# Performance work log

Measured on AMD Instinct MI355X. Metric: run time of the kernel, lower is better.

## Reference

```python
import jax, jax.numpy as jnp
import numpy as np

EPS = 1e-5
B, C_IN, T_IN = 512, 12, 5000
NF, HID, LAT = 32, 64, 32


def setup_inputs() -> dict:
    key = jax.random.key(0)
    ks = jax.random.split(key, 12)
    inp = {
        "x": jax.random.normal(ks[0], (B, C_IN, T_IN), dtype=jnp.float32),
        # conv stack
        "conv1_w": jax.random.normal(ks[1], (32, C_IN, 50), dtype=jnp.float32) * 0.05,
        "conv1_b": jnp.zeros((32,), dtype=jnp.float32),
        "bn1_g": jnp.ones((32,), dtype=jnp.float32),
        "bn1_b": jnp.zeros((32,), dtype=jnp.float32),
        "conv2_w": jax.random.normal(ks[2], (NF, 32, 25), dtype=jnp.float32) * 0.05,
        "conv2_b": jnp.zeros((NF,), dtype=jnp.float32),
        "bn2_g": jnp.ones((NF,), dtype=jnp.float32),
        "bn2_b": jnp.zeros((NF,), dtype=jnp.float32),
        # input projection + layernorm
        "proj_w": jax.random.normal(ks[3], (LAT, NF), dtype=jnp.float32) * 0.1,
        "proj_b": jnp.zeros((LAT,), dtype=jnp.float32),
        "ln_g": jnp.ones((LAT,), dtype=jnp.float32),
        "ln_b": jnp.zeros((LAT,), dtype=jnp.float32),
        # PLRNN recurrence params
        "A": jnp.eye(LAT, dtype=jnp.float32) * 0.9,
        "W": jax.random.normal(ks[4], (LAT, HID), dtype=jnp.float32) * 0.1,
        "h_bias": jnp.zeros((HID,), dtype=jnp.float32),
        # output projection
        "out_w": jax.random.normal(ks[5], (LAT, LAT), dtype=jnp.float32) * 0.1,
        "out_b": jnp.zeros((LAT,), dtype=jnp.float32),
    }
    return inp


def _conv1d(x, w, b, stride):
    # x: [B, C, T], w: [O, I, K]
    y = jax.lax.conv_general_dilated(
        x, w, window_strides=(stride,), padding="VALID",
        dimension_numbers=("NCH", "OIH", "NCH"))
    return y + b[None, :, None]


def _batchnorm_train(x, g, b):
    # training-mode BN over (batch, time) per channel; x: [B, C, T]
    mean = jnp.mean(x, axis=(0, 2), keepdims=True)
    var = jnp.mean((x - mean) ** 2, axis=(0, 2), keepdims=True)
    return (x - mean) * jax.lax.rsqrt(var + EPS) * g[None, :, None] + b[None, :, None]


def _layernorm(x, g, b):
    mean = jnp.mean(x, axis=-1, keepdims=True)
    var = jnp.mean((x - mean) ** 2, axis=-1, keepdims=True)
    return (x - mean) * jax.lax.rsqrt(var + EPS) * g + b


def reference(x, conv1_w, conv1_b, bn1_g, bn1_b, conv2_w, conv2_b, bn2_g, bn2_b,
              proj_w, proj_b, ln_g, ln_b, A, W, h_bias, out_w, out_b):
    # conv front-end
    y = jax.nn.relu(_batchnorm_train(_conv1d(x, conv1_w, conv1_b, 10), bn1_g, bn1_b))
    y = jax.nn.relu(_batchnorm_train(_conv1d(y, conv2_w, conv2_b, 5), bn2_g, bn2_b))
    y = jnp.transpose(y, (0, 2, 1))  # [B, T, NF], T = 95

    # input projection + LN, vectorized over all timesteps
    xt = _layernorm(jnp.einsum("btf,lf->btl", y, proj_w) + proj_b, ln_g, ln_b)  # [B, T, L]
    xs = jnp.transpose(xt, (1, 0, 2))  # [T, B, L] for scan

    def step(h, x_t):
        # h: [B, L]
        linear = h @ A.T
        nonlinear = jax.nn.relu(h @ W + h_bias) @ W.T
        h_new = linear + nonlinear + x_t
        return h_new, h_new

    h0 = jnp.zeros((x.shape[0], A.shape[0]), dtype=x.dtype)
    _, outputs = jax.lax.scan(step, h0, xs)  # [T, B, L]

    pooled = jnp.mean(outputs, axis=0)  # [B, L]
    return pooled @ out_w.T + out_b
```

## Files before the change

kernel.cpp:

```cpp
#include <hip/hip_runtime.h>
#include <stdint.h>

#define NB    512
#define CIN   12
#define TIN   5000
#define T1    496
#define T2    95

#define OFS_STATS 0
#define OFS_W1P   256
#define OFS_W2P   19456
#define OFS_Y1    45056
#define OFS_Y2    8171520

#define GAS __attribute__((address_space(1)))
#define LAS __attribute__((address_space(3)))
#define ASYNC_COPY16(gp, lp) \
    __builtin_amdgcn_global_load_lds((const GAS void*)(gp), (LAS void*)(lp), 16, 0, 0)

__global__ void prep_kernel(const float* __restrict__ w1, const float* __restrict__ w2,
                            float* __restrict__ ws) {
    int idx = blockIdx.x * 256 + threadIdx.x;
    if (idx < 256) ws[idx] = 0.f;
    int j = idx - 256;
    if (j >= 0 && j < 19200) {
        int ic = j / 1600, r = j % 1600, k = r / 32, oc = r % 32;
        ws[OFS_W1P + j] = w1[oc * 600 + ic * 50 + k];
    }
    int j2 = idx - 19456;
    if (j2 >= 0 && j2 < 25600) {
        int ic = j2 / 800, r = j2 % 800, k = r / 32, oc = r % 32;
        ws[OFS_W2P + j2] = w2[oc * 800 + ic * 25 + k];
    }
}

__global__ __launch_bounds__(128, 2) void conv1_kernel(const float* __restrict__ x,
                                                       const float* __restrict__ b1,
                                                       float* __restrict__ ws) {
    const float* w1p = ws + OFS_W1P;
    float* y1 = ws + OFS_Y1;
    float* stats = ws + OFS_STATS;
    int b  = blockIdx.x >> 1;
    int t0 = (blockIdx.x & 1) * 256;
    int tid = threadIdx.x;
    int ocg = tid & 3, tg = tid >> 2;
    int oc0 = ocg * 8;
    int xoff = 10 * tg;

    __shared__ __align__(16) float xs_s[2][2600];
    __shared__ __align__(16) float ws_s[2][1600];
    __shared__ float sred[128];

    float acc[8][8];
#pragma unroll
    for (int a = 0; a < 8; ++a)
#pragma unroll
        for (int c = 0; c < 8; ++c) acc[a][c] = 0.f;

    const float* xb = x + (size_t)b * (CIN * TIN) + t0 * 10;
    const int nchunk = (t0 == 0) ? 650 : 610;
    const int wbase = tid & ~63;

    if (t0 != 0) {
        for (int i = tid; i < 160; i += 128) {
            xs_s[0][2440 + i] = 0.f;
            xs_s[1][2440 + i] = 0.f;
        }
    }

    auto issue = [&](int ic) {
        int buf = ic & 1;
        const float* xg = xb + ic * TIN;
#pragma unroll
        for (int c = 0; c < 6; ++c) {
            int i = c * 128 + tid;
            if (i < nchunk)
                ASYNC_COPY16(xg + 4 * i, &xs_s[buf][4 * (c * 128 + wbase)]);
        }
        const float* wg = w1p + ic * 1600;
#pragma unroll
        for (int c = 0; c < 4; ++c) {
            int i = c * 128 + tid;
            if (i < 400)
                ASYNC_COPY16(wg + 4 * i, &ws_s[buf][4 * (c * 128 + wbase)]);
        }
    };

    issue(0);
    for (int ic = 0; ic < CIN; ++ic) {
        const int cur = ic & 1;
        __syncthreads();
        if (ic + 1 < CIN) issue(ic + 1);

#pragma unroll 1
        for (int m = 0; m < 5; ++m) {
#pragma unroll
            for (int u = 0; u < 5; ++u) {
                const int k = m * 10 + u * 2;
                const float* wr = &ws_s[cur][k * 32 + oc0];
                float4 w00 = *(const float4*)(wr);
                float4 w01 = *(const float4*)(wr + 4);
                float4 w10 = *(const float4*)(wr + 32);
                float4 w11 = *(const float4*)(wr + 36);
                float2 xv[8];
#pragma unroll
                for (int j = 0; j < 8; ++j)
                    xv[j] = *(const float2*)&xs_s[cur][xoff + 320 * j + k];
                float wk[8]  = {w00.x, w00.y, w00.z, w00.w, w01.x, w01.y, w01.z, w01.w};
                float wk1[8] = {w10.x, w10.y, w10.z, w10.w, w11.x, w11.y, w11.z, w11.w};
#pragma unroll
                for (int jo = 0; jo < 8; ++jo)
#pragma unroll
                    for (int j = 0; j < 8; ++j)
                        acc[jo][j] = fmaf(wk1[jo], xv[j].y, fmaf(wk[jo], xv[j].x, acc[jo][j]));
            }
        }
    }

    float bias[8];
#pragma unroll
    for (int jo = 0; jo < 8; ++jo) bias[jo] = b1[oc0 + jo];

    float psum[8], psq[8];
#pragma unroll
    for (int jo = 0; jo < 8; ++jo) { psum[jo] = 0.f; psq[jo] = 0.f; }
#pragma unroll
    for (int jo = 0; jo < 8; ++jo) {
        float* yrow = y1 + (size_t)(b * 32 + oc0 + jo) * T1 + t0 + tg;
#pragma unroll
        for (int j = 0; j < 8; ++j) {
            int trel = tg + 32 * j;
            if (t0 + trel < T1) {
                float v = acc[jo][j] + bias[jo];
                yrow[32 * j] = v;
                psum[jo] += v;
                psq[jo] = fmaf(v, v, psq[jo]);
            }
        }
    }
#pragma unroll
    for (int off = 32; off >= 4; off >>= 1) {
#pragma unroll
        for (int jo = 0; jo < 8; ++jo) {
            psum[jo] += __shfl_down(psum[jo], off, 64);
            psq[jo]  += __shfl_down(psq[jo],  off, 64);
        }
    }
    int lane = tid & 63, wvi = tid >> 6;
    if (lane < 4) {
#pragma unroll
        for (int jo = 0; jo < 8; ++jo) {
            sred[((wvi * 4 + lane) * 8 + jo) * 2 + 0] = psum[jo];
            sred[((wvi * 4 + lane) * 8 + jo) * 2 + 1] = psq[jo];
        }
    }
    __syncthreads();
    if (tid < 64) {
        int oc = tid >> 1, which = tid & 1;
        int og = oc >> 3, jo = oc & 7;
        float v = sred[((0 * 4 + og) * 8 + jo) * 2 + which] +
                  sred[((1 * 4 + og) * 8 + jo) * 2 + which];
        atomicAdd(&stats[which * 32 + oc], v);
    }
}

__global__ __launch_bounds__(256, 2) void conv2bn_kernel(const float* __restrict__ g1,
                                                         const float* __restrict__ be1,
                                                         const float* __restrict__ b2,
                                                         float* __restrict__ ws) {
    const float* w2p = ws + OFS_W2P;
    const float* y1 = ws + OFS_Y1;
    float* y2 = ws + OFS_Y2;
    float* stats = ws + OFS_STATS;
    int b = blockIdx.x, tid = threadIdx.x;
    int ocg = tid & 7, tg = tid >> 3;
    int oc0 = ocg * 4;

    __shared__ float s1s[32], sh1s[32];
    __shared__ __align__(16) float a1s[512];
    __shared__ __align__(16) float w2s[800];
    __shared__ float sred[256];

    float acc[4][3];
#pragma unroll
    for (int a = 0; a < 4; ++a)
#pragma unroll
        for (int c = 0; c < 3; ++c) acc[a][c] = 0.f;

    if (tid < 32) {
        float mean = stats[tid] * (1.f / 253952.f);
        float var  = stats[32 + tid] * (1.f / 253952.f) - mean * mean;
        float s = g1[tid] * rsqrtf(var + 1e-5f);
        s1s[tid] = s;
        sh1s[tid] = be1[tid] - mean * s;
    }

    float4 pa, pw2;
    auto fetch = [&](int ic) {
        if (tid < 124) pa  = *(const float4*)(y1 + (size_t)(b * 32 + ic) * T1 + 4 * tid);
        if (tid < 200) pw2 = *(const float4*)(w2p + ic * 800 + 4 * tid);
    };
    fetch(0);
    __syncthreads();

#pragma unroll 1
    for (int ic = 0; ic < 32; ++ic) {
        float s1 = s1s[ic], sh1 = sh1s[ic];
        if (tid < 124) {
            float4 v = pa;
            v.x = fmaxf(fmaf(v.x, s1, sh1), 0.f);
            v.y = fmaxf(fmaf(v.y, s1, sh1), 0.f);
            v.z = fmaxf(fmaf(v.z, s1, sh1), 0.f);
            v.w = fmaxf(fmaf(v.w, s1, sh1), 0.f);
            *(float4*)&a1s[4 * tid] = v;
        }
        if (tid < 200) *(float4*)&w2s[4 * tid] = pw2;
        if (ic + 1 < 32) fetch(ic + 1);
        __builtin_amdgcn_sched_barrier(0);
        __syncthreads();

#pragma unroll
        for (int kp = 0; kp < 12; ++kp) {
            const int k = kp * 2;
            float4 wA = *(const float4*)&w2s[k * 32 + oc0];
            float4 wB = *(const float4*)&w2s[(k + 1) * 32 + oc0];
            float x0[3], x1[3];
#pragma unroll
            for (int jt = 0; jt < 3; ++jt) {
                int a = 15 * tg + 5 * jt + k;
                x0[jt] = a1s[a]; x1[jt] = a1s[a + 1];
            }
            float wk[4]  = {wA.x, wA.y, wA.z, wA.w};
            float wk1[4] = {wB.x, wB.y, wB.z, wB.w};
#pragma unroll
            for (int jo = 0; jo < 4; ++jo)
#pragma unroll
                for (int jt = 0; jt < 3; ++jt)
                    acc[jo][jt] = fmaf(wk1[jo], x1[jt], fmaf(wk[jo], x0[jt], acc[jo][jt]));
        }
        {
            float4 wT = *(const float4*)&w2s[24 * 32 + oc0];
            float wt[4] = {wT.x, wT.y, wT.z, wT.w};
#pragma unroll
            for (int jt = 0; jt < 3; ++jt) {
                float xt_ = a1s[15 * tg + 5 * jt + 24];
#pragma unroll
                for (int jo = 0; jo < 4; ++jo) acc[jo][jt] = fmaf(wt[jo], xt_, acc[jo][jt]);
            }
        }
        __syncthreads();
    }

    float bias[4];
#pragma unroll
    for (int jo = 0; jo < 4; ++jo) bias[jo] = b2[oc0 + jo];

    float psum[4], psq[4];
#pragma unroll
    for (int jo = 0; jo < 4; ++jo) {
        float s = 0.f, q = 0.f;
#pragma unroll
        for (int jt = 0; jt < 3; ++jt) {
            int t2 = 3 * tg + jt;
            if (t2 < T2) {
                float v = acc[jo][jt] + bias[jo];
                y2[(size_t)b * 3040 + (oc0 + jo) * T2 + t2] = v;
                s += v; q = fmaf(v, v, q);
            }
        }
        psum[jo] = s; psq[jo] = q;
    }
#pragma unroll
    for (int off = 32; off >= 8; off >>= 1) {
#pragma unroll
        for (int jo = 0; jo < 4; ++jo) {
            psum[jo] += __shfl_down(psum[jo], off, 64);
            psq[jo]  += __shfl_down(psq[jo],  off, 64);
        }
    }
    int lane = tid & 63, wvi = tid >> 6;
    if (lane < 8) {
#pragma unroll
        for (int jo = 0; jo < 4; ++jo) {
            sred[((wvi * 8 + lane) * 4 + jo) * 2 + 0] = psum[jo];
            sred[((wvi * 8 + lane) * 4 + jo) * 2 + 1] = psq[jo];
        }
    }
    __syncthreads();
    if (tid < 64) {
        int oc = tid >> 1, which = tid & 1;
        int og = oc >> 2, jo = oc & 3;
        float v = 0.f;
#pragma unroll
        for (int w = 0; w < 4; ++w)
            v += sred[((w * 8 + og) * 4 + jo) * 2 + which];
        atomicAdd(&stats[64 + which * 32 + oc], v);
    }
}

__global__ __launch_bounds__(256, 2) void projscan_kernel(const float* __restrict__ g2,
                                                          const float* __restrict__ be2,
                                                          const float* __restrict__ pw,
                                                          const float* __restrict__ pb,
                                                          const float* __restrict__ lng,
                                                          const float* __restrict__ lnb,
                                                          const float* __restrict__ Am,
                                                          const float* __restrict__ Wm,
                                                          const float* __restrict__ hbp,
                                                          const float* __restrict__ ow,
                                                          const float* __restrict__ ob,
                                                          const float* __restrict__ ws,
                                                          float* __restrict__ out) {
    int b = blockIdx.x, tid = threadIdx.x;
    __shared__ float s2s[32], sh2s[32];
    __shared__ __align__(16) float a2s[3040];
    __shared__ float pws[1056], ows[1056];
    __shared__ __align__(16) float xsl[3135];
    __shared__ __align__(16) float hs[32];
    __shared__ __align__(16) float hds[64];
    const float* stats = ws + OFS_STATS;
    const float* y2b = ws + OFS_Y2 + (size_t)b * 3040;

    if (tid < 32) {
        float mean = stats[64 + tid] * (1.f / 48640.f);
        float var  = stats[96 + tid] * (1.f / 48640.f) - mean * mean;
        float s = g2[tid] * rsqrtf(var + 1e-5f);
        s2s[tid] = s;
        sh2s[tid] = be2[tid] - mean * s;
    }
    for (int i = tid; i < 1024; i += 256) {
        pws[(i >> 5) * 33 + (i & 31)] = pw[i];
        ows[(i >> 5) * 33 + (i & 31)] = ow[i];
    }
    __syncthreads();

    for (int i = tid; i < 760; i += 256) {
        float4 v = *(const float4*)(y2b + 4 * i);
        float r[4] = {v.x, v.y, v.z, v.w};
        float o[4];
#pragma unroll
        for (int e = 0; e < 4; ++e) {
            int idx = 4 * i + e;
            int oc = idx / 95;
            o[e] = fmaxf(fmaf(r[e], s2s[oc], sh2s[oc]), 0.f);
        }
        float4 vv; vv.x = o[0]; vv.y = o[1]; vv.z = o[2]; vv.w = o[3];
        *(float4*)&a2s[4 * i] = vv;
    }
    __syncthreads();

    int l = tid & 31, ts = tid >> 5;
    {
        float pbv = pb[l], lg = lng[l], lb = lnb[l];
        for (int it = 0; it < 12; ++it) {
            int t = ts + 8 * it;
            if (t < T2) {
                float v = pbv;
#pragma unroll
                for (int f = 0; f < 32; ++f)
                    v = fmaf(a2s[f * T2 + t], pws[l * 33 + f], v);
                float sum = v;
#pragma unroll
                for (int off = 16; off >= 1; off >>= 1) sum += __shfl_xor(sum, off, 64);
                float mean = sum * (1.f / 32.f);
                float d = v - mean;
                float q = d * d;
#pragma unroll
                for (int off = 16; off >= 1; off >>= 1) q += __shfl_xor(q, off, 64);
                float o = d * rsqrtf(q * (1.f / 32.f) + 1e-5f) * lg + lb;
                xsl[t * 33 + l] = o;
            }
        }
    }
    __syncthreads();

    if (tid < 64) {
        int lane = tid, half = lane >> 5;
        float Wc[32], WT[32], Ah[16];
#pragma unroll
        for (int j = 0; j < 32; ++j) Wc[j] = Wm[j * 64 + lane];
#pragma unroll
        for (int m = 0; m < 32; ++m) WT[m] = Wm[l * 64 + half * 32 + m];
#pragma unroll
        for (int j = 0; j < 16; ++j) Ah[j] = Am[l * 32 + half * 16 + j];
        float hbv = hbp[lane];
        if (lane < 32) hs[l] = 0.f;
        float xv = xsl[l];
        float pool = 0.f;

        for (int t = 0; t < T2; ++t) {
            float4 hv[8];
#pragma unroll
            for (int q = 0; q < 8; ++q) hv[q] = *(const float4*)&hs[4 * q];
            float a0 = hbv, a1 = 0.f, a2 = 0.f, a3 = 0.f;
#pragma unroll
            for (int q = 0; q < 8; ++q) {
                a0 = fmaf(Wc[4 * q + 0], hv[q].x, a0);
                a1 = fmaf(Wc[4 * q + 1], hv[q].y, a1);
                a2 = fmaf(Wc[4 * q + 2], hv[q].z, a2);
                a3 = fmaf(Wc[4 * q + 3], hv[q].w, a3);
            }
            float hid = fmaxf((a0 + a1) + (a2 + a3), 0.f);
            float4 hl[4];
#pragma unroll
            for (int q = 0; q < 4; ++q) hl[q] = *(const float4*)&hs[half * 16 + 4 * q];
            float l0 = 0.f, l1 = 0.f;
#pragma unroll
            for (int q = 0; q < 4; ++q) {
                l0 = fmaf(Ah[4 * q + 0], hl[q].x, l0);
                l1 = fmaf(Ah[4 * q + 1], hl[q].y, l1);
                l0 = fmaf(Ah[4 * q + 2], hl[q].z, l0);
                l1 = fmaf(Ah[4 * q + 3], hl[q].w, l1);
            }
            float lin = l0 + l1;
            hds[lane] = hid;
            float n0 = 0.f, n1 = 0.f, n2 = 0.f, n3 = 0.f;
#pragma unroll
            for (int q = 0; q < 8; ++q) {
                float4 d4 = *(const float4*)&hds[half * 32 + 4 * q];
                n0 = fmaf(WT[4 * q + 0], d4.x, n0);
                n1 = fmaf(WT[4 * q + 1], d4.y, n1);
                n2 = fmaf(WT[4 * q + 2], d4.z, n2);
                n3 = fmaf(WT[4 * q + 3], d4.w, n3);
            }
            float part = (n0 + n1) + (n2 + n3) + lin;
            part += __shfl_xor(part, 32, 64);
            float hnew = part + xv;
            pool += hnew;
            if (t + 1 < T2) xv = xsl[(t + 1) * 33 + l];
            if (lane < 32) hs[l] = hnew;
        }

        if (lane < 32) hs[l] = pool * (1.f / 95.f);
        if (lane < 32) {
            float4 p0 = *(const float4*)&hs[0];
            float4 p1 = *(const float4*)&hs[4];
            float4 p2 = *(const float4*)&hs[8];
            float4 p3 = *(const float4*)&hs[12];
            float4 p4 = *(const float4*)&hs[16];
            float4 p5 = *(const float4*)&hs[20];
            float4 p6 = *(const float4*)&hs[24];
            float4 p7 = *(const float4*)&hs[28];
            float o = ob[l];
            const float* owr = &ows[l * 33];
            o = fmaf(owr[0],  p0.x, o); o = fmaf(owr[1],  p0.y, o);
            o = fmaf(owr[2],  p0.z, o); o = fmaf(owr[3],  p0.w, o);
            o = fmaf(owr[4],  p1.x, o); o = fmaf(owr[5],  p1.y, o);
            o = fmaf(owr[6],  p1.z, o); o = fmaf(owr[7],  p1.w, o);
            o = fmaf(owr[8],  p2.x, o); o = fmaf(owr[9],  p2.y, o);
            o = fmaf(owr[10], p2.z, o); o = fmaf(owr[11], p2.w, o);
            o = fmaf(owr[12], p3.x, o); o = fmaf(owr[13], p3.y, o);
            o = fmaf(owr[14], p3.z, o); o = fmaf(owr[15], p3.w, o);
            o = fmaf(owr[16], p4.x, o); o = fmaf(owr[17], p4.y, o);
            o = fmaf(owr[18], p4.z, o); o = fmaf(owr[19], p4.w, o);
            o = fmaf(owr[20], p5.x, o); o = fmaf(owr[21], p5.y, o);
            o = fmaf(owr[22], p5.z, o); o = fmaf(owr[23], p5.w, o);
            o = fmaf(owr[24], p6.x, o); o = fmaf(owr[25], p6.y, o);
            o = fmaf(owr[26], p6.z, o); o = fmaf(owr[27], p6.w, o);
            o = fmaf(owr[28], p7.x, o); o = fmaf(owr[29], p7.y, o);
            o = fmaf(owr[30], p7.z, o); o = fmaf(owr[31], p7.w, o);
            out[b * 32 + l] = o;
        }
    }
}

extern "C" void kernel_launch(void* const* d_in, const int* in_sizes, int n_in,
                              void* d_out, int out_size, void* d_ws, size_t ws_size,
                              hipStream_t stream) {
    (void)in_sizes; (void)n_in; (void)out_size; (void)ws_size;
    const float* x   = (const float*)d_in[0];
    const float* w1  = (const float*)d_in[1];
    const float* b1  = (const float*)d_in[2];
    const float* g1  = (const float*)d_in[3];
    const float* be1 = (const float*)d_in[4];
    const float* w2  = (const float*)d_in[5];
    const float* b2  = (const float*)d_in[6];
    const float* g2  = (const float*)d_in[7];
    const float* be2 = (const float*)d_in[8];
    const float* pw  = (const float*)d_in[9];
    const float* pb  = (const float*)d_in[10];
    const float* lng = (const float*)d_in[11];
    const float* lnb = (const float*)d_in[12];
    const float* Am  = (const float*)d_in[13];
    const float* Wm  = (const float*)d_in[14];
    const float* hb  = (const float*)d_in[15];
    const float* ow  = (const float*)d_in[16];
    const float* ob  = (const float*)d_in[17];
    float* ws  = (float*)d_ws;
    float* out = (float*)d_out;

    prep_kernel<<<176, 256, 0, stream>>>(w1, w2, ws);
    conv1_kernel<<<1024, 128, 0, stream>>>(x, b1, ws);
    conv2bn_kernel<<<512, 256, 0, stream>>>(g1, be1, b2, ws);
    projscan_kernel<<<512, 256, 0, stream>>>(g2, be2, pw, pb, lng, lnb,
                                             Am, Wm, hb, ow, ob, ws, out);
}
```

Before: 498.8 us.

## Restructure conv kernels to per-thread time columns with uniform scalar weight loads

Both conv kernels now give each thread one or two time positions and all 32 output channels. Weights are no longer staged through LDS; they are read directly from global memory with wave-uniform addresses that the compiler can turn into scalar loads. conv2 drops to 128 threads, uses async global-to-LDS copies for the input rows, and reduces BN statistics with full-wave shuffles. This removes LDS weight traffic and bank pressure but raises register use (64 accumulators plus 64 partial sums), leaves about a quarter of the threads idle in conv2, and adds more shuffle work.

Measured after the change: 841.9 us. 68.8% more time.

```diff
diff --git a/kernel.cpp b/kernel.cpp
--- a/kernel.cpp
+++ b/kernel.cpp
@@ -37,36 +37,23 @@
 __global__ __launch_bounds__(128, 2) void conv1_kernel(const float* __restrict__ x,
                                                        const float* __restrict__ b1,
                                                        float* __restrict__ ws) {
-    const float* w1p = ws + OFS_W1P;
+    const float* __restrict__ w1p = ws + OFS_W1P;
     float* y1 = ws + OFS_Y1;
     float* stats = ws + OFS_STATS;
     int b  = blockIdx.x >> 1;
     int t0 = (blockIdx.x & 1) * 256;
     int tid = threadIdx.x;
-    int ocg = tid & 3, tg = tid >> 2;
-    int oc0 = ocg * 8;
-    int xoff = 10 * tg;
 
     __shared__ __align__(16) float xs_s[2][2600];
-    __shared__ __align__(16) float ws_s[2][1600];
     __shared__ float sred[128];
 
-    float acc[8][8];
-#pragma unroll
-    for (int a = 0; a < 8; ++a)
-#pragma unroll
-        for (int c = 0; c < 8; ++c) acc[a][c] = 0.f;
+    float acc[32][2];
+#pragma unroll
+    for (int oc = 0; oc < 32; ++oc) { acc[oc][0] = 0.f; acc[oc][1] = 0.f; }
 
     const float* xb = x + (size_t)b * (CIN * TIN) + t0 * 10;
     const int nchunk = (t0 == 0) ? 650 : 610;
     const int wbase = tid & ~63;
-
-    if (t0 != 0) {
-        for (int i = tid; i < 160; i += 128) {
-            xs_s[0][2440 + i] = 0.f;
-            xs_s[1][2440 + i] = 0.f;
-        }
-    }
 
     auto issue = [&](int ic) {
         int buf = ic & 1;
@@ -76,13 +63,6 @@
             int i = c * 128 + tid;
             if (i < nchunk)
                 ASYNC_COPY16(xg + 4 * i, &xs_s[buf][4 * (c * 128 + wbase)]);
-        }
-        const float* wg = w1p + ic * 1600;
-#pragma unroll
-        for (int c = 0; c < 4; ++c) {
-            int i = c * 128 + tid;
-            if (i < 400)
-                ASYNC_COPY16(wg + 4 * i, &ws_s[buf][4 * (c * 128 + wbase)]);
         }
     };
 
@@ -91,101 +71,78 @@
         const int cur = ic & 1;
         __syncthreads();
         if (ic + 1 < CIN) issue(ic + 1);
-
+        const float* __restrict__ wrow = w1p + ic * 1600;
+        const int x0 = 10 * tid;
 #pragma unroll 1
-        for (int m = 0; m < 5; ++m) {
-#pragma unroll
-            for (int u = 0; u < 5; ++u) {
-                const int k = m * 10 + u * 2;
-                const float* wr = &ws_s[cur][k * 32 + oc0];
-                float4 w00 = *(const float4*)(wr);
-                float4 w01 = *(const float4*)(wr + 4);
-                float4 w10 = *(const float4*)(wr + 32);
-                float4 w11 = *(const float4*)(wr + 36);
-                float2 xv[8];
-#pragma unroll
-                for (int j = 0; j < 8; ++j)
-                    xv[j] = *(const float2*)&xs_s[cur][xoff + 320 * j + k];
-                float wk[8]  = {w00.x, w00.y, w00.z, w00.w, w01.x, w01.y, w01.z, w01.w};
-                float wk1[8] = {w10.x, w10.y, w10.z, w10.w, w11.x, w11.y, w11.z, w11.w};
-#pragma unroll
-                for (int jo = 0; jo < 8; ++jo)
-#pragma unroll
-                    for (int j = 0; j < 8; ++j)
-                        acc[jo][j] = fmaf(wk1[jo], xv[j].y, fmaf(wk[jo], xv[j].x, acc[jo][j]));
+        for (int kp = 0; kp < 25; ++kp) {
+            const int k = kp * 2;
+            float2 xv0 = *(const float2*)&xs_s[cur][x0 + k];
+            float2 xv1 = *(const float2*)&xs_s[cur][x0 + 1280 + k];
+            const float* __restrict__ wk = wrow + k * 32;
+#pragma unroll
+            for (int oc = 0; oc < 32; ++oc) {
+                float w0 = wk[oc];
+                float w1v = wk[32 + oc];
+                acc[oc][0] = fmaf(w1v, xv0.y, fmaf(w0, xv0.x, acc[oc][0]));
+                acc[oc][1] = fmaf(w1v, xv1.y, fmaf(w0, xv1.x, acc[oc][1]));
             }
         }
     }
 
-    float bias[8];
-#pragma unroll
-    for (int jo = 0; jo < 8; ++jo) bias[jo] = b1[oc0 + jo];
-
-    float psum[8], psq[8];
-#pragma unroll
-    for (int jo = 0; jo < 8; ++jo) { psum[jo] = 0.f; psq[jo] = 0.f; }
-#pragma unroll
-    for (int jo = 0; jo < 8; ++jo) {
-        float* yrow = y1 + (size_t)(b * 32 + oc0 + jo) * T1 + t0 + tg;
-#pragma unroll
-        for (int j = 0; j < 8; ++j) {
-            int trel = tg + 32 * j;
-            if (t0 + trel < T1) {
-                float v = acc[jo][j] + bias[jo];
-                yrow[32 * j] = v;
-                psum[jo] += v;
-                psq[jo] = fmaf(v, v, psq[jo]);
-            }
-        }
-    }
-#pragma unroll
-    for (int off = 32; off >= 4; off >>= 1) {
-#pragma unroll
-        for (int jo = 0; jo < 8; ++jo) {
-            psum[jo] += __shfl_down(psum[jo], off, 64);
-            psq[jo]  += __shfl_down(psq[jo],  off, 64);
-        }
-    }
-    int lane = tid & 63, wvi = tid >> 6;
-    if (lane < 4) {
-#pragma unroll
-        for (int jo = 0; jo < 8; ++jo) {
-            sred[((wvi * 4 + lane) * 8 + jo) * 2 + 0] = psum[jo];
-            sred[((wvi * 4 + lane) * 8 + jo) * 2 + 1] = psq[jo];
+    bool v1 = (t0 + 128 + tid) < T1;
+    float psum[32], psq[32];
+#pragma unroll
+    for (int oc = 0; oc < 32; ++oc) {
+        float bi = b1[oc];
+        float a0 = acc[oc][0] + bi;
+        float a1v = acc[oc][1] + bi;
+        float* yr = y1 + (size_t)(b * 32 + oc) * T1 + t0 + tid;
+        yr[0] = a0;
+        float s = a0, q = a0 * a0;
+        if (v1) { yr[128] = a1v; s += a1v; q = fmaf(a1v, a1v, q); }
+        psum[oc] = s; psq[oc] = q;
+    }
+#pragma unroll
+    for (int off = 32; off >= 1; off >>= 1) {
+#pragma unroll
+        for (int oc = 0; oc < 32; ++oc) {
+            psum[oc] += __shfl_down(psum[oc], off, 64);
+            psq[oc]  += __shfl_down(psq[oc],  off, 64);
+        }
+    }
+    int lane = tid & 63, wv = tid >> 6;
+    if (lane == 0) {
+#pragma unroll
+        for (int oc = 0; oc < 32; ++oc) {
+            sred[wv * 64 + oc * 2 + 0] = psum[oc];
+            sred[wv * 64 + oc * 2 + 1] = psq[oc];
         }
     }
     __syncthreads();
     if (tid < 64) {
         int oc = tid >> 1, which = tid & 1;
-        int og = oc >> 3, jo = oc & 7;
-        float v = sred[((0 * 4 + og) * 8 + jo) * 2 + which] +
-                  sred[((1 * 4 + og) * 8 + jo) * 2 + which];
+        float v = sred[tid] + sred[64 + tid];
         atomicAdd(&stats[which * 32 + oc], v);
     }
 }
 
-__global__ __launch_bounds__(256, 2) void conv2bn_kernel(const float* __restrict__ g1,
+__global__ __launch_bounds__(128, 2) void conv2bn_kernel(const float* __restrict__ g1,
                                                          const float* __restrict__ be1,
                                                          const float* __restrict__ b2,
                                                          float* __restrict__ ws) {
-    const float* w2p = ws + OFS_W2P;
+    const float* __restrict__ w2p = ws + OFS_W2P;
     const float* y1 = ws + OFS_Y1;
     float* y2 = ws + OFS_Y2;
     float* stats = ws + OFS_STATS;
     int b = blockIdx.x, tid = threadIdx.x;
-    int ocg = tid & 7, tg = tid >> 3;
-    int oc0 = ocg * 4;
 
     __shared__ float s1s[32], sh1s[32];
-    __shared__ __align__(16) float a1s[512];
-    __shared__ __align__(16) float w2s[800];
-    __shared__ float sred[256];
-
-    float acc[4][3];
-#pragma unroll
-    for (int a = 0; a < 4; ++a)
-#pragma unroll
-        for (int c = 0; c < 3; ++c) acc[a][c] = 0.f;
+    __shared__ __align__(16) float a1s[2][496];
+    __shared__ float sred[128];
+
+    float acc[32];
+#pragma unroll
+    for (int oc = 0; oc < 32; ++oc) acc[oc] = 0.f;
 
     if (tid < 32) {
         float mean = stats[tid] * (1.f / 253952.f);
@@ -195,105 +152,73 @@
         sh1s[tid] = be1[tid] - mean * s;
     }
 
-    float4 pa, pw2;
-    auto fetch = [&](int ic) {
-        if (tid < 124) pa  = *(const float4*)(y1 + (size_t)(b * 32 + ic) * T1 + 4 * tid);
-        if (tid < 200) pw2 = *(const float4*)(w2p + ic * 800 + 4 * tid);
+    const int wbase = tid & ~63;
+    auto issue = [&](int ic) {
+        int buf = ic & 1;
+        const float* yg = y1 + (size_t)(b * 32 + ic) * T1;
+        if (tid < 124)
+            ASYNC_COPY16(yg + 4 * tid, &a1s[buf][4 * wbase]);
     };
-    fetch(0);
-    __syncthreads();
-
-#pragma unroll 1
+
+    issue(0);
+    const int tt = (tid < T2) ? tid : 0;
     for (int ic = 0; ic < 32; ++ic) {
+        const int cur = ic & 1;
+        __syncthreads();
         float s1 = s1s[ic], sh1 = sh1s[ic];
         if (tid < 124) {
-            float4 v = pa;
+            float4 v = *(const float4*)&a1s[cur][4 * tid];
             v.x = fmaxf(fmaf(v.x, s1, sh1), 0.f);
             v.y = fmaxf(fmaf(v.y, s1, sh1), 0.f);
             v.z = fmaxf(fmaf(v.z, s1, sh1), 0.f);
             v.w = fmaxf(fmaf(v.w, s1, sh1), 0.f);
-            *(float4*)&a1s[4 * tid] = v;
-        }
-        if (tid < 200) *(float4*)&w2s[4 * tid] = pw2;
-        if (ic + 1 < 32) fetch(ic + 1);
-        __builtin_amdgcn_sched_barrier(0);
+            *(float4*)&a1s[cur][4 * tid] = v;
+        }
         __syncthreads();
-
-#pragma unroll
-        for (int kp = 0; kp < 12; ++kp) {
-            const int k = kp * 2;
-            float4 wA = *(const float4*)&w2s[k * 32 + oc0];
-            float4 wB = *(const float4*)&w2s[(k + 1) * 32 + oc0];
-            float x0[3], x1[3];
-#pragma unroll
-            for (int jt = 0; jt < 3; ++jt) {
-                int a = 15 * tg + 5 * jt + k;
-                x0[jt] = a1s[a]; x1[jt] = a1s[a + 1];
-            }
-            float wk[4]  = {wA.x, wA.y, wA.z, wA.w};
-            float wk1[4] = {wB.x, wB.y, wB.z, wB.w};
-#pragma unroll
-            for (int jo = 0; jo < 4; ++jo)
-#pragma unroll
-                for (int jt = 0; jt < 3; ++jt)
-                    acc[jo][jt] = fmaf(wk1[jo], x1[jt], fmaf(wk[jo], x0[jt], acc[jo][jt]));
-        }
-        {
-            float4 wT = *(const float4*)&w2s[24 * 32 + oc0];
-            float wt[4] = {wT.x, wT.y, wT.z, wT.w};
-#pragma unroll
-            for (int jt = 0; jt < 3; ++jt) {
-                float xt_ = a1s[15 * tg + 5 * jt + 24];
-#pragma unroll
-                for (int jo = 0; jo < 4; ++jo) acc[jo][jt] = fmaf(wt[jo], xt_, acc[jo][jt]);
-            }
-        }
-        __syncthreads();
-    }
-
-    float bias[4];
-#pragma unroll
-    for (int jo = 0; jo < 4; ++jo) bias[jo] = b2[oc0 + jo];
-
-    float psum[4], psq[4];
-#pragma unroll
-    for (int jo = 0; jo < 4; ++jo) {
-        float s = 0.f, q = 0.f;
-#pragma unroll
-        for (int jt = 0; jt < 3; ++jt) {
-            int t2 = 3 * tg + jt;
-            if (t2 < T2) {
-                float v = acc[jo][jt] + bias[jo];
-                y2[(size_t)b * 3040 + (oc0 + jo) * T2 + t2] = v;
-                s += v; q = fmaf(v, v, q);
-            }
-        }
-        psum[jo] = s; psq[jo] = q;
-    }
-#pragma unroll
-    for (int off = 32; off >= 8; off >>= 1) {
-#pragma unroll
-        for (int jo = 0; jo < 4; ++jo) {
-            psum[jo] += __shfl_down(psum[jo], off, 64);
-            psq[jo]  += __shfl_down(psq[jo],  off, 64);
-        }
-    }
-    int lane = tid & 63, wvi = tid >> 6;
-    if (lane < 8) {
-#pragma unroll
-        for (int jo = 0; jo < 4; ++jo) {
-            sred[((wvi * 8 + lane) * 4 + jo) * 2 + 0] = psum[jo];
-            sred[((wvi * 8 + lane) * 4 + jo) * 2 + 1] = psq[jo];
+        if (ic + 1 < 32) issue(ic + 1);
+
+        const float* __restrict__ wrow = w2p + ic * 800;
+        const int xbase = 5 * tt;
+#pragma unroll 5
+        for (int k = 0; k < 25; ++k) {
+            float xv = a1s[cur][xbase + k];
+            const float* __restrict__ wk = wrow + k * 32;
+#pragma unroll
+            for (int oc = 0; oc < 32; ++oc)
+                acc[oc] = fmaf(wk[oc], xv, acc[oc]);
+        }
+    }
+
+    bool valid = tid < T2;
+    float psum[32], psq[32];
+#pragma unroll
+    for (int oc = 0; oc < 32; ++oc) {
+        float v = acc[oc] + b2[oc];
+        if (valid) {
+            y2[(size_t)b * 3040 + oc * T2 + tid] = v;
+            psum[oc] = v; psq[oc] = v * v;
+        } else { psum[oc] = 0.f; psq[oc] = 0.f; }
+    }
+#pragma unroll
+    for (int off = 32; off >= 1; off >>= 1) {
+#pragma unroll
+        for (int oc = 0; oc < 32; ++oc) {
+            psum[oc] += __shfl_down(psum[oc], off, 64);
+            psq[oc]  += __shfl_down(psq[oc],  off, 64);
+        }
+    }
+    int lane = tid & 63, wv = tid >> 6;
+    if (lane == 0) {
+#pragma unroll
+        for (int oc = 0; oc < 32; ++oc) {
+            sred[wv * 64 + oc * 2 + 0] = psum[oc];
+            sred[wv * 64 + oc * 2 + 1] = psq[oc];
         }
     }
     __syncthreads();
     if (tid < 64) {
         int oc = tid >> 1, which = tid & 1;
-        int og = oc >> 2, jo = oc & 3;
-        float v = 0.f;
-#pragma unroll
-        for (int w = 0; w < 4; ++w)
-            v += sred[((w * 8 + og) * 4 + jo) * 2 + which];
+        float v = sred[tid] + sred[64 + tid];
         atomicAdd(&stats[64 + which * 32 + oc], v);
     }
 }
@@ -491,7 +416,7 @@
 
     prep_kernel<<<176, 256, 0, stream>>>(w1, w2, ws);
     conv1_kernel<<<1024, 128, 0, stream>>>(x, b1, ws);
-    conv2bn_kernel<<<512, 256, 0, stream>>>(g1, be1, b2, ws);
+    conv2bn_kernel<<<512, 128, 0, stream>>>(g1, be1, b2, ws);
     projscan_kernel<<<512, 256, 0, stream>>>(g2, be2, pw, pb, lng, lnb,
                                              Am, Wm, hb, ow, ob, ws, out);
 }
```
